# Kernel optimization log

Hardware: AMD Instinct MI355X
Metric: run time of the kernel (lower is better)

The kernel has to match this reference:

```python
import jax, jax.numpy as jnp
import numpy as np

FACTOR = 5


def setup_inputs() -> dict:
    key = jax.random.key(0)
    k1, k2, k3, k4, k5 = jax.random.split(key, 5)
    B, L, H, D = 4, 2048, 8, 64
    queries = jax.random.normal(k1, (B, L, H, D), dtype=jnp.float32)
    keys = jax.random.normal(k2, (B, L, H, D), dtype=jnp.float32)
    values = jax.random.normal(k3, (B, L, H, D), dtype=jnp.float32)
    his_timeslot = jnp.sort(jax.random.uniform(k4, (B, L), dtype=jnp.float32), axis=-1)
    label_pre_timeslot = jax.random.uniform(k5, (B, L), dtype=jnp.float32)
    attn_mask = jnp.zeros((1,), dtype=bool)
    return {"queries": queries, "keys": keys, "values": values,
            "his_timeslot": his_timeslot, "label_pre_timeslot": label_pre_timeslot,
            "attn_mask": attn_mask}


def _forward(queries, keys, values, his_timeslot):
    B, L_Q, H, D = queries.shape
    L_K = keys.shape[1]
    # torch .view(B, H, L, -1) is a reshape of the contiguous buffer, NOT a transpose
    Q = queries.reshape(B, H, L_Q, D)
    K = keys.reshape(B, H, L_K, D)
    V = values.reshape(B, H, L_K, D)

    sample_k = FACTOR * int(np.ceil(np.log(L_K)))   # U_part
    n_top = FACTOR * int(np.ceil(np.log(L_Q)))      # u

    # --- _prob_QK: random key sampling + sparsity measure + top-k queries ---
    skey = jax.random.key(42)
    index_sample = jax.random.randint(skey, (L_Q, sample_k), 0, L_K)  # [L_Q, S]
    K_sample = K[:, :, index_sample, :]                               # [B,H,L_Q,S,E]
    Q_K_sample = jnp.einsum('bhie,bhise->bhis', Q, K_sample)          # [B,H,L_Q,S]
    M = Q_K_sample.max(axis=-1) - Q_K_sample.sum(axis=-1) / L_K       # [B,H,L_Q]
    _, M_top = jax.lax.top_k(M, n_top)                                # [B,H,u]

    # Continuous-time pairwise score: 0.5 * (Q_sel_i . K_j + Q_j . K_sel_i)
    idx = M_top[..., None]
    Q_sel = jnp.take_along_axis(Q, jnp.broadcast_to(idx, (B, H, n_top, D)), axis=2)
    K_sel = jnp.take_along_axis(K, jnp.broadcast_to(idx, (B, H, n_top, D)), axis=2)
    scores = 0.5 * (jnp.einsum('bhue,bhle->bhul', Q_sel, K)
                    + jnp.einsum('bhle,bhue->bhul', Q, K_sel))        # [B,H,u,L_K]
    scale = 1.0 / np.sqrt(D)
    scores = scores * scale

    # --- initial context: triangular sum over pairwise trapezoid of V ---
    # CT_values[b,h,i,j,d] = 0.5*(V_i + V_j); context_i = sum_{j<=i} CT_values[i,j]
    coef = (jnp.arange(L_K, dtype=V.dtype) + 1.0)[:, None]            # (i+1)
    context = 0.5 * (coef * V + jnp.cumsum(V, axis=2))                # [B,H,L_K,D]

    # --- ProbMask (causal for selected queries) + softmax ---
    causal = jnp.triu(jnp.ones((L_Q, L_K), dtype=bool), k=1)          # j > i
    prob_mask = causal[M_top]                                         # [B,H,u,L_K]
    attn = jax.nn.softmax(jnp.where(prob_mask, -1e9, scores), axis=-1)

    # sum_j attn[i,j] * 0.5*(V[M_top_i] + V_j) = 0.5*(V_sel + attn @ V)
    V_sel = jnp.take_along_axis(V, jnp.broadcast_to(idx, (B, H, n_top, D)), axis=2)
    updated = 0.5 * (V_sel + jnp.einsum('bhul,bhld->bhud', attn, V))  # [B,H,u,D]

    bidx = jnp.arange(B)[:, None, None]
    hidx = jnp.arange(H)[None, :, None]
    context = context.at[bidx, hidx, M_top].set(updated)
    return context.transpose(0, 2, 1, 3)                              # [B,L,H,D]


def reference(queries, keys, values, his_timeslot, label_pre_timeslot, attn_mask):
    return _forward(queries, keys, values, his_timeslot)
```

## Files before the change

kernel.cpp:

```cpp
#include <hip/hip_runtime.h>
#include <stdint.h>
#include <math.h>

#define Bn 4
#define Ln 2048
#define Hn 8
#define Dn 64
#define BHn (Bn*Hn)
#define NTOP 40
#define SK   40
#define NSAMP (Ln*SK)

__host__ __device__ inline uint32_t rotl32(uint32_t x, int r) {
  return (x << r) | (x >> (32 - r));
}

__host__ __device__ inline void tf2x32(uint32_t k0, uint32_t k1,
                                       uint32_t& x0, uint32_t& x1) {
  const uint32_t ks2 = k0 ^ k1 ^ 0x1BD11BDAu;
  const int RA[4] = {13, 15, 26, 6};
  const int RB[4] = {17, 29, 16, 24};
  x0 += k0; x1 += k1;
  for (int i = 0; i < 4; i++) { x0 += x1; x1 = rotl32(x1, RA[i]); x1 ^= x0; }
  x0 += k1;  x1 += ks2 + 1u;
  for (int i = 0; i < 4; i++) { x0 += x1; x1 = rotl32(x1, RB[i]); x1 ^= x0; }
  x0 += ks2; x1 += k0 + 2u;
  for (int i = 0; i < 4; i++) { x0 += x1; x1 = rotl32(x1, RA[i]); x1 ^= x0; }
  x0 += k0;  x1 += k1 + 3u;
  for (int i = 0; i < 4; i++) { x0 += x1; x1 = rotl32(x1, RB[i]); x1 ^= x0; }
  x0 += k1;  x1 += ks2 + 4u;
  for (int i = 0; i < 4; i++) { x0 += x1; x1 = rotl32(x1, RA[i]); x1 ^= x0; }
  x0 += ks2; x1 += k0 + 5u;
}

__device__ inline int draw2048(uint32_t k0, uint32_t k1, uint32_t n) {
  uint32_t a = 0u, b = n;
  tf2x32(k0, k1, a, b);
  return (int)((a ^ b) & (Ln - 1));
}

template<int CTRL>
__device__ __forceinline__ float dpp_add(float x) {
  int y = __builtin_amdgcn_update_dpp(0, __float_as_int(x), CTRL, 0xF, 0xF, true);
  return x + __int_as_float(y);
}
__device__ __forceinline__ float red16(float d) {
  d = dpp_add<0xB1>(d);
  d = dpp_add<0x4E>(d);
  d = dpp_add<0x141>(d);
  d = dpp_add<0x140>(d);
  return d;
}

__global__ __launch_bounds__(256) void fused_m_vsum(const float* __restrict__ Q,
                                                    const float* __restrict__ K,
                                                    const float* __restrict__ V,
                                                    float* __restrict__ M,
                                                    float* __restrict__ partial,
                                                    uint32_t k0, uint32_t k1) {
  __shared__ alignas(16) int sidx[16][40];
  __shared__ float red[4][64];

  if (blockIdx.x < 1024) {
    int bid  = blockIdx.x;
    int tile = bid & 31;
    int bh   = bid >> 5;
    int d = threadIdx.x & 63;
    int g = threadIdx.x >> 6;
    const float* Vb = V + (size_t)bh * Ln * Dn;
    int l0 = tile * 64 + g * 16;
    float s = 0.f;
    for (int j = 0; j < 16; j++) s += Vb[(size_t)(l0 + j) * Dn + d];
    red[g][d] = s;
    __syncthreads();
    if (g == 0)
      partial[((size_t)bh * 32 + tile) * 64 + d] =
          red[0][d] + red[1][d] + red[2][d] + red[3][d];
    return;
  }

  int cmb = blockIdx.x - 1024;
  int xcd = cmb & 7;
  int idx = cmb >> 3;
  int bh  = (idx & 3) * 8 + xcd;
  int seg = idx >> 2;
  int tid = threadIdx.x;
  int qw  = tid >> 4;
  int j   = tid & 15;
  int i   = seg * 16 + qw;

  uint32_t n0 = (uint32_t)(i * SK);
  sidx[qw][j]      = draw2048(k0, k1, n0 + j);
  sidx[qw][16 + j] = draw2048(k0, k1, n0 + 16 + j);
  if (j < 8) sidx[qw][32 + j] = draw2048(k0, k1, n0 + 32 + j);

  const float* Qb = Q + ((size_t)bh * Ln + i) * Dn;
  float4 qf = ((const float4*)Qb)[j];
  __syncthreads();

  int4 I[10];
#pragma unroll
  for (int t = 0; t < 10; t++) I[t] = *(const int4*)&sidx[qw][t * 4];

  const float* Kb = K + (size_t)bh * Ln * Dn;
  float mx = -INFINITY, sm = 0.f;
#pragma unroll
  for (int t = 0; t < 10; t++) {
    int ls[4] = {I[t].x, I[t].y, I[t].z, I[t].w};
#pragma unroll
    for (int c = 0; c < 4; c++) {
      float4 kf = ((const float4*)(Kb + (size_t)ls[c] * Dn))[j];
      float d = qf.x * kf.x + qf.y * kf.y + qf.z * kf.z + qf.w * kf.w;
      d = red16(d);
      mx = fmaxf(mx, d);
      sm += d;
    }
  }
  if (j == 0)
    M[(size_t)bh * Ln + i] = mx - sm * (1.0f / (float)Ln);
}

__global__ __launch_bounds__(256) void fused_topk_ctx(const float* __restrict__ M,
                                                      int* __restrict__ Mtop,
                                                      const float* __restrict__ V,
                                                      const float* __restrict__ partial,
                                                      float* __restrict__ out) {
  __shared__ float cv[4][NTOP];
  __shared__ int   ci[4][NTOP];
  __shared__ float red[4][64];

  if (blockIdx.x < 32) {
    int bh = blockIdx.x;
    int tid = threadIdx.x, lane = tid & 63, w = tid >> 6;
    {
      float cur[8];
      const float* m = M + (size_t)bh * Ln + w * 512;
#pragma unroll
      for (int j = 0; j < 8; j++) cur[j] = m[lane + 64 * j];
      for (int k = 0; k < NTOP; ++k) {
        float bv = cur[0]; int bj = 0;
#pragma unroll
        for (int j = 1; j < 8; j++)
          if (cur[j] > bv) { bv = cur[j]; bj = j; }
        int bi = w * 512 + lane + 64 * bj;
#pragma unroll
        for (int off = 1; off < 64; off <<= 1) {
          float ov = __shfl_xor(bv, off, 64);
          int   oi = __shfl_xor(bi, off, 64);
          if (ov > bv || (ov == bv && oi < bi)) { bv = ov; bi = oi; }
        }
        if (lane == 0) { cv[w][k] = bv; ci[w][k] = bi; }
        int ll  = bi & 63;
        int jj = (bi - w * 512) >> 6;
        if (lane == ll) cur[jj] = -INFINITY;
      }
    }
    __syncthreads();
    if (w == 0) {
      float cur[3]; int gix[3];
#pragma unroll
      for (int j = 0; j < 3; j++) {
        int c = lane + 64 * j;
        if (c < 160) { cur[j] = cv[c / NTOP][c % NTOP]; gix[j] = ci[c / NTOP][c % NTOP]; }
        else         { cur[j] = -INFINITY; gix[j] = 0x7fffffff; }
      }
      for (int k = 0; k < NTOP; ++k) {
        float bv = cur[0]; int bg = gix[0];
#pragma unroll
        for (int j = 1; j < 3; j++)
          if (cur[j] > bv || (cur[j] == bv && gix[j] < bg)) { bv = cur[j]; bg = gix[j]; }
#pragma unroll
        for (int off = 1; off < 64; off <<= 1) {
          float ov = __shfl_xor(bv, off, 64);
          int   og = __shfl_xor(bg, off, 64);
          if (ov > bv || (ov == bv && og < bg)) { bv = ov; bg = og; }
        }
        if (lane == 0) Mtop[bh * NTOP + k] = bg;
#pragma unroll
        for (int j = 0; j < 3; j++)
          if (gix[j] == bg) cur[j] = -INFINITY;
      }
    }
    return;
  }

  int bid  = blockIdx.x - 32;
  int tile = bid & 31;
  int bh   = bid >> 5;
  int b = bh >> 3, h = bh & 7;
  int d = threadIdx.x & 63;
  int g = threadIdx.x >> 6;
  float p = 0.f;
  for (int t = g; t < tile; t += 4)
    p += partial[((size_t)bh * 32 + t) * 64 + d];
  red[g][d] = p;
  __syncthreads();
  float prefix = red[0][d] + red[1][d] + red[2][d] + red[3][d];
  __syncthreads();
  const float* Vb = V + (size_t)bh * Ln * Dn;
  int l0 = tile * 64 + g * 16;
  float vloc[16]; float s = 0.f;
  for (int j = 0; j < 16; j++) {
    vloc[j] = Vb[(size_t)(l0 + j) * Dn + d];
    s += vloc[j];
  }
  red[g][d] = s;
  __syncthreads();
  float running = prefix;
  for (int gg = 0; gg < g; gg++) running += red[gg][d];
  for (int j = 0; j < 16; j++) {
    int l = l0 + j;
    running += vloc[j];
    out[(((size_t)b * Ln + l) * Hn + h) * Dn + d] =
        0.5f * ((float)(l + 1) * vloc[j] + running);
  }
}

#define UC 5
__global__ __launch_bounds__(512, 2) void sparse_attn(const float* __restrict__ Q,
                                                      const float* __restrict__ K,
                                                      const float* __restrict__ V,
                                                      const int* __restrict__ Mtop,
                                                      float* __restrict__ out) {
  int xcd  = blockIdx.x & 7;
  int rest = blockIdx.x >> 3;
  int chunk = rest & 7;
  int bh    = (rest >> 3) * 8 + xcd;
  int b = bh >> 3, h = bh & 7;
  __shared__ alignas(16) float sc[UC][Ln];
  __shared__ alignas(16) float qs[UC][Dn];
  __shared__ alignas(16) float ks[UC][Dn];
  __shared__ float vs[UC][Dn];
  __shared__ alignas(16) float redp[8][UC][64];
  __shared__ int   rows_s[UC];
  __shared__ float inv_s[UC];
  const float* Qb = Q + (size_t)bh * Ln * Dn;
  const float* Kb = K + (size_t)bh * Ln * Dn;
  const float* Vb = V + (size_t)bh * Ln * Dn;
  int tid = threadIdx.x;

  if (tid < UC * 64) {
    int u = tid >> 6, d = tid & 63;
    int row = Mtop[bh * NTOP + chunk * UC + u];
    if (d == 0) rows_s[u] = row;
    qs[u][d] = Qb[(size_t)row * Dn + d];
    ks[u][d] = Kb[(size_t)row * Dn + d];
    vs[u][d] = Vb[(size_t)row * Dn + d];
  }
  __syncthreads();

  float acc[UC][4];
#pragma unroll
  for (int u = 0; u < UC; u++)
#pragma unroll
    for (int j = 0; j < 4; j++) acc[u][j] = 0.f;

  for (int tt = 0; tt < 4; tt++) {
    float4 kk[4][4], qq[4][4];
#pragma unroll
    for (int j = 0; j < 4; j++) {
      int l = tid + j * 512;
      const float4* kp = (const float4*)(Kb + (size_t)l * Dn) + tt * 4;
      const float4* qp = (const float4*)(Qb + (size_t)l * Dn) + tt * 4;
#pragma unroll
      for (int ts = 0; ts < 4; ts++) { kk[j][ts] = kp[ts]; qq[j][ts] = qp[ts]; }
    }
#pragma unroll
    for (int ts = 0; ts < 4; ts++) {
      int t = tt * 4 + ts;
#pragma unroll
      for (int u = 0; u < UC; u++) {
        float4 q4 = *(const float4*)(&qs[u][t * 4]);
        float4 k4 = *(const float4*)(&ks[u][t * 4]);
#pragma unroll
        for (int j = 0; j < 4; j++) {
          acc[u][j] += q4.x * kk[j][ts].x + q4.y * kk[j][ts].y
                     + q4.z * kk[j][ts].z + q4.w * kk[j][ts].w
                     + k4.x * qq[j][ts].x + k4.y * qq[j][ts].y
                     + k4.z * qq[j][ts].z + k4.w * qq[j][ts].w;
        }
      }
    }
  }
#pragma unroll
  for (int u = 0; u < UC; u++) {
    int row = rows_s[u];
#pragma unroll
    for (int j = 0; j < 4; j++) {
      int l = tid + j * 512;
      sc[u][l] = (l > row) ? -1e9f : acc[u][j] * 0.0625f;
    }
  }
  __syncthreads();

  int w = tid >> 6, lane = tid & 63;
  if (w < UC) {
    float mx = -INFINITY;
    for (int kq = 0; kq < 32; kq++) mx = fmaxf(mx, sc[w][lane + 64 * kq]);
    for (int off = 32; off; off >>= 1) mx = fmaxf(mx, __shfl_xor(mx, off, 64));
    float sum = 0.f;
    for (int kq = 0; kq < 32; kq++) {
      float e = __expf(sc[w][lane + 64 * kq] - mx);
      sc[w][lane + 64 * kq] = e;
      sum += e;
    }
    for (int off = 32; off; off >>= 1) sum += __shfl_xor(sum, off, 64);
    if (lane == 0) inv_s[w] = 1.0f / sum;
  }
  __syncthreads();

  {
    int quad = lane & 15, lr = lane >> 4;
    int l0w = w * 256;
    const float4* V4 = (const float4*)Vb;
    float4 a[UC];
#pragma unroll
    for (int u = 0; u < UC; u++) a[u] = make_float4(0.f, 0.f, 0.f, 0.f);
    for (int it4 = 0; it4 < 16; it4++) {
      int lb = l0w + lr + it4 * 16;
      float4 v0 = V4[(size_t)(lb)      * 16 + quad];
      float4 v1 = V4[(size_t)(lb + 4)  * 16 + quad];
      float4 v2 = V4[(size_t)(lb + 8)  * 16 + quad];
      float4 v3 = V4[(size_t)(lb + 12) * 16 + quad];
#pragma unroll
      for (int u = 0; u < UC; u++) {
        float s0 = sc[u][lb], s1 = sc[u][lb + 4], s2 = sc[u][lb + 8], s3 = sc[u][lb + 12];
        a[u].x += s0 * v0.x + s1 * v1.x + s2 * v2.x + s3 * v3.x;
        a[u].y += s0 * v0.y + s1 * v1.y + s2 * v2.y + s3 * v3.y;
        a[u].z += s0 * v0.z + s1 * v1.z + s2 * v2.z + s3 * v3.z;
        a[u].w += s0 * v0.w + s1 * v1.w + s2 * v2.w + s3 * v3.w;
      }
    }
#pragma unroll
    for (int u = 0; u < UC; u++) {
#pragma unroll
      for (int off = 16; off < 64; off <<= 1) {
        a[u].x += __shfl_xor(a[u].x, off, 64);
        a[u].y += __shfl_xor(a[u].y, off, 64);
        a[u].z += __shfl_xor(a[u].z, off, 64);
        a[u].w += __shfl_xor(a[u].w, off, 64);
      }
      if (lr == 0) *(float4*)(&redp[w][u][quad * 4]) = a[u];
    }
  }
  __syncthreads();

  if (w < UC) {
    float r = 0.f;
#pragma unroll
    for (int g = 0; g < 8; g++) r += redp[g][w][lane];
    float outv = 0.5f * (vs[w][lane] + r * inv_s[w]);
    int row = rows_s[w];
    out[(((size_t)b * Ln + row) * Hn + h) * Dn + lane] = outv;
  }
}

extern "C" void kernel_launch(void* const* d_in, const int* in_sizes, int n_in,
                              void* d_out, int out_size, void* d_ws, size_t ws_size,
                              hipStream_t stream) {
  const float* Q = (const float*)d_in[0];
  const float* K = (const float*)d_in[1];
  const float* V = (const float*)d_in[2];
  float* out = (float*)d_out;
  char* ws = (char*)d_ws;

  float* M       = (float*)(ws + NSAMP * 4);
  int*   Mtop    = (int*)(ws + NSAMP * 4 + BHn * Ln * 4);
  float* partial = (float*)(ws + NSAMP * 4 + BHn * Ln * 4 + BHn * NTOP * 4);

  uint32_t s0 = 0u, s1 = 1u;
  tf2x32(0u, 42u, s0, s1);

  fused_m_vsum<<<1024 + 4096, 256, 0, stream>>>(Q, K, V, M, partial, s0, s1);
  fused_topk_ctx<<<32 + 1024, 256, 0, stream>>>(M, Mtop, V, partial, out);
  sparse_attn<<<BHn * 8, 512, 0, stream>>>(Q, K, V, Mtop, out);
}
```

Baseline: 216.5 us.

## Use radix-threshold top-k and fuse context cumsum into sparse attention kernel

Replaces the iterative 40-round shuffle-based top-k with a bitwise binary search on order-preserving float keys, which counts elements at or above a threshold and then gathers the winners with ties broken by lowest index. The cumulative-sum context write moves out of the top-k kernel and into extra blocks of the sparse attention kernel. Those blocks skip rows that the sparse path overwrites, so the two kernels no longer race on the same output rows. The intent is to shorten the serial top-k critical path and let the context writes overlap with the attention work. In exchange, the top-k becomes a tiny 32-block launch and the order of the indices it writes is no longer sorted.

```diff
diff --git a/kernel.cpp b/kernel.cpp
--- a/kernel.cpp
+++ b/kernel.cpp
@@ -120,113 +120,87 @@
     M[(size_t)bh * Ln + i] = mx - sm * (1.0f / (float)Ln);
 }
 
-__global__ __launch_bounds__(256) void fused_topk_ctx(const float* __restrict__ M,
-                                                      int* __restrict__ Mtop,
-                                                      const float* __restrict__ V,
-                                                      const float* __restrict__ partial,
-                                                      float* __restrict__ out) {
-  __shared__ float cv[4][NTOP];
-  __shared__ int   ci[4][NTOP];
-  __shared__ float red[4][64];
-
-  if (blockIdx.x < 32) {
-    int bh = blockIdx.x;
-    int tid = threadIdx.x, lane = tid & 63, w = tid >> 6;
-    {
-      float cur[8];
-      const float* m = M + (size_t)bh * Ln + w * 512;
-#pragma unroll
-      for (int j = 0; j < 8; j++) cur[j] = m[lane + 64 * j];
-      for (int k = 0; k < NTOP; ++k) {
-        float bv = cur[0]; int bj = 0;
-#pragma unroll
-        for (int j = 1; j < 8; j++)
-          if (cur[j] > bv) { bv = cur[j]; bj = j; }
-        int bi = w * 512 + lane + 64 * bj;
-#pragma unroll
-        for (int off = 1; off < 64; off <<= 1) {
-          float ov = __shfl_xor(bv, off, 64);
-          int   oi = __shfl_xor(bi, off, 64);
-          if (ov > bv || (ov == bv && oi < bi)) { bv = ov; bi = oi; }
-        }
-        if (lane == 0) { cv[w][k] = bv; ci[w][k] = bi; }
-        int ll  = bi & 63;
-        int jj = (bi - w * 512) >> 6;
-        if (lane == ll) cur[jj] = -INFINITY;
-      }
-    }
-    __syncthreads();
-    if (w == 0) {
-      float cur[3]; int gix[3];
-#pragma unroll
-      for (int j = 0; j < 3; j++) {
-        int c = lane + 64 * j;
-        if (c < 160) { cur[j] = cv[c / NTOP][c % NTOP]; gix[j] = ci[c / NTOP][c % NTOP]; }
-        else         { cur[j] = -INFINITY; gix[j] = 0x7fffffff; }
-      }
-      for (int k = 0; k < NTOP; ++k) {
-        float bv = cur[0]; int bg = gix[0];
-#pragma unroll
-        for (int j = 1; j < 3; j++)
-          if (cur[j] > bv || (cur[j] == bv && gix[j] < bg)) { bv = cur[j]; bg = gix[j]; }
-#pragma unroll
-        for (int off = 1; off < 64; off <<= 1) {
-          float ov = __shfl_xor(bv, off, 64);
-          int   og = __shfl_xor(bg, off, 64);
-          if (ov > bv || (ov == bv && og < bg)) { bv = ov; bg = og; }
-        }
-        if (lane == 0) Mtop[bh * NTOP + k] = bg;
-#pragma unroll
-        for (int j = 0; j < 3; j++)
-          if (gix[j] == bg) cur[j] = -INFINITY;
-      }
-    }
-    return;
-  }
-
-  int bid  = blockIdx.x - 32;
-  int tile = bid & 31;
-  int bh   = bid >> 5;
-  int b = bh >> 3, h = bh & 7;
-  int d = threadIdx.x & 63;
-  int g = threadIdx.x >> 6;
-  float p = 0.f;
-  for (int t = g; t < tile; t += 4)
-    p += partial[((size_t)bh * 32 + t) * 64 + d];
-  red[g][d] = p;
-  __syncthreads();
-  float prefix = red[0][d] + red[1][d] + red[2][d] + red[3][d];
-  __syncthreads();
-  const float* Vb = V + (size_t)bh * Ln * Dn;
-  int l0 = tile * 64 + g * 16;
-  float vloc[16]; float s = 0.f;
-  for (int j = 0; j < 16; j++) {
-    vloc[j] = Vb[(size_t)(l0 + j) * Dn + d];
-    s += vloc[j];
-  }
-  red[g][d] = s;
-  __syncthreads();
-  float running = prefix;
-  for (int gg = 0; gg < g; gg++) running += red[gg][d];
-  for (int j = 0; j < 16; j++) {
-    int l = l0 + j;
-    running += vloc[j];
-    out[(((size_t)b * Ln + l) * Hn + h) * Dn + d] =
-        0.5f * ((float)(l + 1) * vloc[j] + running);
+__global__ __launch_bounds__(256) void topk_select(const float* __restrict__ M,
+                                                   int* __restrict__ Mtop) {
+  int bh = blockIdx.x;
+  int tid = threadIdx.x;
+  const float* m = M + (size_t)bh * Ln;
+
+  uint32_t k[8]; int li[8];
+  float4 va = ((const float4*)m)[tid * 2];
+  float4 vb = ((const float4*)m)[tid * 2 + 1];
+  float vals[8] = {va.x, va.y, va.z, va.w, vb.x, vb.y, vb.z, vb.w};
+#pragma unroll
+  for (int j = 0; j < 8; j++) {
+    uint32_t u = __float_as_uint(vals[j]);
+    k[j] = (u & 0x80000000u) ? ~u : (u | 0x80000000u);
+    li[j] = tid * 8 + j;
+  }
+
+  __shared__ int cnts[32];
+  __shared__ int cA, outc, eqn2;
+  __shared__ int eqbuf[2048];
+  if (tid < 32) cnts[tid] = 0;
+  if (tid == 0) { cA = 0; outc = 0; eqn2 = 0; }
+  __syncthreads();
+
+  uint32_t lo = 0u, hi = 0xFFFFFFFFu;
+  for (int it = 0; it < 32; ++it) {
+    if (lo >= hi) break;
+    uint32_t mid = lo + ((hi - lo) >> 1) + 1u;
+    int cw = 0;
+#pragma unroll
+    for (int j = 0; j < 8; j++)
+      cw += __popcll(__ballot(k[j] >= mid));
+    if ((tid & 63) == 0) atomicAdd(&cnts[it], cw);
+    __syncthreads();
+    int total = cnts[it];
+    if (total >= NTOP) lo = mid; else hi = mid - 1u;
+  }
+  uint32_t K40 = lo;
+
+  {
+    int cw = 0;
+#pragma unroll
+    for (int j = 0; j < 8; j++)
+      cw += __popcll(__ballot(k[j] > K40));
+    if ((tid & 63) == 0) atomicAdd(&cA, cw);
+  }
+  __syncthreads();
+
+#pragma unroll
+  for (int j = 0; j < 8; j++) {
+    if (k[j] > K40) {
+      int p = atomicAdd(&outc, 1);
+      Mtop[bh * NTOP + p] = li[j];
+    } else if (k[j] == K40) {
+      int p = atomicAdd(&eqn2, 1);
+      eqbuf[p] = li[j];
+    }
+  }
+  __syncthreads();
+
+  if (tid == 0) {
+    int need = NTOP - cA;
+    int n = eqn2;
+    for (int s = 0; s < need; s++) {
+      int best = 0x7fffffff, bi = 0;
+      for (int t = 0; t < n; t++)
+        if (eqbuf[t] < best) { best = eqbuf[t]; bi = t; }
+      Mtop[bh * NTOP + cA + s] = best;
+      eqbuf[bi] = 0x7fffffff;
+    }
   }
 }
 
 #define UC 5
-__global__ __launch_bounds__(512, 2) void sparse_attn(const float* __restrict__ Q,
-                                                      const float* __restrict__ K,
-                                                      const float* __restrict__ V,
-                                                      const int* __restrict__ Mtop,
-                                                      float* __restrict__ out) {
-  int xcd  = blockIdx.x & 7;
-  int rest = blockIdx.x >> 3;
-  int chunk = rest & 7;
-  int bh    = (rest >> 3) * 8 + xcd;
-  int b = bh >> 3, h = bh & 7;
+#define SPB 256
+__global__ __launch_bounds__(512, 2) void sparse_ctx(const float* __restrict__ Q,
+                                                     const float* __restrict__ K,
+                                                     const float* __restrict__ V,
+                                                     const int* __restrict__ Mtop,
+                                                     const float* __restrict__ partial,
+                                                     float* __restrict__ out) {
   __shared__ alignas(16) float sc[UC][Ln];
   __shared__ alignas(16) float qs[UC][Dn];
   __shared__ alignas(16) float ks[UC][Dn];
@@ -234,6 +208,56 @@
   __shared__ alignas(16) float redp[8][UC][64];
   __shared__ int   rows_s[UC];
   __shared__ float inv_s[UC];
+  __shared__ alignas(16) float credR[8][64];
+  __shared__ uint32_t cmask[64];
+
+  if (blockIdx.x >= SPB) {
+    int bid = blockIdx.x - SPB;
+    int bh  = bid >> 4;
+    int T   = bid & 15;
+    int b = bh >> 3, h = bh & 7;
+    int tid = threadIdx.x, d = tid & 63, g = tid >> 6;
+    if (tid < 64) cmask[tid] = 0u;
+    __syncthreads();
+    if (tid < NTOP) {
+      int r = Mtop[bh * NTOP + tid];
+      atomicOr(&cmask[r >> 5], 1u << (r & 31));
+    }
+    float p = 0.f;
+    for (int t = g; t < 2 * T; t += 8)
+      p += partial[((size_t)bh * 32 + t) * 64 + d];
+    credR[g][d] = p;
+    __syncthreads();
+    float prefix = 0.f;
+#pragma unroll
+    for (int gg = 0; gg < 8; gg++) prefix += credR[gg][d];
+    __syncthreads();
+    const float* Vb = V + (size_t)bh * Ln * Dn;
+    int l0 = T * 128 + g * 16;
+    float vloc[16]; float s = 0.f;
+    for (int j = 0; j < 16; j++) {
+      vloc[j] = Vb[(size_t)(l0 + j) * Dn + d];
+      s += vloc[j];
+    }
+    credR[g][d] = s;
+    __syncthreads();
+    float running = prefix;
+    for (int gg = 0; gg < g; gg++) running += credR[gg][d];
+    for (int j = 0; j < 16; j++) {
+      int l = l0 + j;
+      running += vloc[j];
+      if (!((cmask[l >> 5] >> (l & 31)) & 1u))
+        out[(((size_t)b * Ln + l) * Hn + h) * Dn + d] =
+            0.5f * ((float)(l + 1) * vloc[j] + running);
+    }
+    return;
+  }
+
+  int xcd  = blockIdx.x & 7;
+  int rest = blockIdx.x >> 3;
+  int chunk = rest & 7;
+  int bh    = (rest >> 3) * 8 + xcd;
+  int b = bh >> 3, h = bh & 7;
   const float* Qb = Q + (size_t)bh * Ln * Dn;
   const float* Kb = K + (size_t)bh * Ln * Dn;
   const float* Vb = V + (size_t)bh * Ln * Dn;
@@ -372,6 +396,6 @@
   tf2x32(0u, 42u, s0, s1);
 
   fused_m_vsum<<<1024 + 4096, 256, 0, stream>>>(Q, K, V, M, partial, s0, s1);
-  fused_topk_ctx<<<32 + 1024, 256, 0, stream>>>(M, Mtop, V, partial, out);
-  sparse_attn<<<BHn * 8, 512, 0, stream>>>(Q, K, V, Mtop, out);
-}
+  topk_select<<<BHn, 256, 0, stream>>>(M, Mtop);
+  sparse_ctx<<<SPB + 512, 512, 0, stream>>>(Q, K, V, Mtop, partial, out);
+}
```

Result: faster. 180.7 us (-16.5%).
